# Kernel optimization log

Hardware: AMD Instinct MI355X
Metric: run time of the kernel (lower is better)

The kernel has to match this reference:

```python
import jax, jax.numpy as jnp
import numpy as np

B, L, D = 2, 2048, 2048
HQ, HKV = 32, 8
HD = D // HQ            # 64
G = HQ // HKV           # 4


def setup_inputs() -> dict:
    key = jax.random.key(0)
    ks = jax.random.split(key, 9)
    s = 1.0 / np.sqrt(D)
    return {
        "x": jax.random.normal(ks[0], (B, L, D), jnp.float32),
        "Wq": jax.random.normal(ks[1], (D, HQ * HD), jnp.float32) * s,
        "bq": jnp.zeros((HQ * HD,), jnp.float32),
        "Wk": jax.random.normal(ks[2], (D, HKV * HD), jnp.float32) * s,
        "bk": jnp.zeros((HKV * HD,), jnp.float32),
        "Wv": jax.random.normal(ks[3], (D, HKV * HD), jnp.float32) * s,
        "bv": jnp.zeros((HKV * HD,), jnp.float32),
        "Wo": jax.random.normal(ks[4], (HQ * HD, D), jnp.float32) * s,
        "bo": jnp.zeros((D,), jnp.float32),
    }


def reference(x, Wq, bq, Wk, bk, Wv, bv, Wo, bo):
    # projections
    q = x @ Wq + bq                                   # [B, L, HQ*HD]
    k = x @ Wk + bk                                   # [B, L, HKV*HD]
    v = x @ Wv + bv
    # split heads; group q heads by kv head: [B, HKV, G, L, HD]
    q = q.reshape(B, L, HKV, G, HD).transpose(0, 2, 3, 1, 4)
    k = k.reshape(B, L, HKV, HD).transpose(0, 2, 1, 3)   # [B, HKV, L, HD]
    v = v.reshape(B, L, HKV, HD).transpose(0, 2, 1, 3)
    scale = 1.0 / np.sqrt(HD)
    # scores [B, HKV, G, Lq, Lk] -- same math as repeat_kv + matmul
    scores = jnp.einsum('bhgqd,bhkd->bhgqk', q, k) * scale
    attn = jax.nn.softmax(scores, axis=-1)
    ctx = jnp.einsum('bhgqk,bhkd->bhgqd', attn, v)       # [B, HKV, G, L, HD]
    # merge heads back to [B, L, HQ*HD]
    ctx = ctx.transpose(0, 3, 1, 2, 4).reshape(B, L, HQ * HD)
    return ctx @ Wo + bo
```

## Files before the change

### kernel.cpp

```cpp
#include <hip/hip_runtime.h>
#include <cstdint>
#include <cstring>


#define L_SEQ 2048
#define D_MODEL 2048
#define M_ROWS 4096
#define KV_COLS 512
#define ATTN_SCALE 0.18033688011112042f

typedef __bf16 bf16x8 __attribute__((ext_vector_type(8)));
typedef float f32x4 __attribute__((ext_vector_type(4)));
typedef float f32x16 __attribute__((ext_vector_type(16)));

__device__ __forceinline__ f32x4 zero4() {
    f32x4 v; v[0] = 0.f; v[1] = 0.f; v[2] = 0.f; v[3] = 0.f; return v;
}

__device__ __forceinline__ unsigned short f2bf(float x) {
    unsigned u = __builtin_bit_cast(unsigned, x);
    u = (u + 0x7FFFu + ((u >> 16) & 1u)) >> 16;
    return (unsigned short)u;
}

__device__ __forceinline__ unsigned pk_bf16(float a, float b) {
#if __has_builtin(__builtin_amdgcn_cvt_pk_bf16_f32)
    typedef __bf16 bf16x2 __attribute__((ext_vector_type(2)));
    bf16x2 r = __builtin_amdgcn_cvt_pk_bf16_f32(a, b);
    return __builtin_bit_cast(unsigned, r);
#else
    return (unsigned)f2bf(a) | ((unsigned)f2bf(b) << 16);
#endif
}

__device__ __forceinline__ f32x4 mfma16(uint4 a, uint4 b, f32x4 c) {
    return __builtin_amdgcn_mfma_f32_16x16x32_bf16(
        __builtin_bit_cast(bf16x8, a), __builtin_bit_cast(bf16x8, b), c, 0, 0, 0);
}
__device__ __forceinline__ f32x16 mfma32(uint4 a, uint4 b, f32x16 c) {
    return __builtin_amdgcn_mfma_f32_32x32x16_bf16(
        __builtin_bit_cast(bf16x8, a), __builtin_bit_cast(bf16x8, b), c, 0, 0, 0);
}

__device__ __forceinline__ void gl_lds16(const unsigned short* g, unsigned short* l) {
    __builtin_amdgcn_global_load_lds(
        (const __attribute__((address_space(1))) unsigned int*)g,
        (__attribute__((address_space(3))) unsigned int*)l, 16, 0, 0);
}

#if __has_builtin(__builtin_amdgcn_exp2f)
#define EXP2F(x) __builtin_amdgcn_exp2f(x)
#else
#define EXP2F(x) exp2f(x)
#endif

__device__ __forceinline__ void permswap32(unsigned& a, unsigned& b) {
    asm("v_permlane32_swap_b32 %0, %1" : "+v"(a), "+v"(b));
}


__global__ __launch_bounds__(256) void cast_x_kernel(const float* __restrict__ in,
                                                     unsigned short* __restrict__ out,
                                                     int n4) {
    int i = blockIdx.x * 256 + threadIdx.x;
    if (i >= n4) return;
    float4 v = ((const float4*)in)[i];
    uint2 o;
    o.x = pk_bf16(v.x, v.y);
    o.y = pk_bf16(v.z, v.w);
    ((uint2*)out)[i] = o;
}

__global__ __launch_bounds__(256) void transpose_cast_kernel(const float* __restrict__ in,
                                                             unsigned short* __restrict__ out,
                                                             int N, int row_off) {
    __shared__ float tile[32][33];
    const int n0 = blockIdx.x * 32, k0 = blockIdx.y * 32;
    const int tc = threadIdx.x & 31, tr = threadIdx.x >> 5;
#pragma unroll
    for (int i = 0; i < 4; ++i)
        tile[tr + i * 8][tc] = in[(size_t)(k0 + tr + i * 8) * N + n0 + tc];
    __syncthreads();
#pragma unroll
    for (int i = 0; i < 4; ++i)
        out[(size_t)(row_off + n0 + tr + i * 8) * 2048 + k0 + tc] = f2bf(tile[tc][tr + i * 8]);
}

__global__ __launch_bounds__(256) void transpose_v_kernel(const unsigned short* __restrict__ Vb,
                                                          unsigned short* __restrict__ Vt) {
    __shared__ unsigned short tile[32][33];
    const int c0 = blockIdx.x * 32, l0 = blockIdx.y * 32, b = blockIdx.z;
    const int tc = threadIdx.x & 31, tr = threadIdx.x >> 5;
#pragma unroll
    for (int i = 0; i < 4; ++i)
        tile[tr + i * 8][tc] = Vb[(size_t)(b * 2048 + l0 + tr + i * 8) * KV_COLS + c0 + tc];
    __syncthreads();
#pragma unroll
    for (int i = 0; i < 4; ++i)
        Vt[(size_t)(b * 512 + c0 + tr + i * 8) * 2048 + l0 + tc] = tile[tc][tr + i * 8];
}


__device__ __forceinline__ void gemm_ring_core(const unsigned short* __restrict__ A,
                                               const unsigned short* __restrict__ Bt,
                                               int arow0, int brow0,
                                               char* smem, f32x4 acc[4][2]) {
    const int tid = threadIdx.x;
    const int w = tid >> 6, lane = tid & 63;
    const int wm = w >> 2, wn = w & 3;
    const int lr = lane & 15, lg = lane >> 4;
    const int rr = lane >> 3, cp = lane & 7;

#pragma unroll
    for (int i = 0; i < 4; ++i)
#pragma unroll
        for (int j = 0; j < 2; ++j) acc[i][j] = zero4();

    auto stage = [&](int kt, int slot) {
        char* base = smem + slot * 32768;
        const int k8 = kt * 64 + ((cp ^ rr) * 8);
#pragma unroll
        for (int s = 0; s < 2; ++s) {
            const int c = w * 2 + s;
            gl_lds16(A + (size_t)(arow0 + c * 8 + rr) * 2048 + k8,
                     (unsigned short*)(base + c * 1024));
            gl_lds16(Bt + (size_t)(brow0 + c * 8 + rr) * 2048 + k8,
                     (unsigned short*)(base + 16384 + c * 1024));
        }
    };

    stage(0, 0);
    stage(1, 1);

    for (int t = 0; t < 32; ++t) {
        if (t < 31) asm volatile("s_waitcnt vmcnt(4)" ::: "memory");
        else        asm volatile("s_waitcnt vmcnt(0)" ::: "memory");
        __builtin_amdgcn_s_barrier();
        asm volatile("" ::: "memory");

        if (t <= 29) stage(t + 2, (t + 2) % 3);

        const char* Ab = smem + (t % 3) * 32768;
        const char* Bb = Ab + 16384;

        uint4 fa[4][2], fb[2][2];
#pragma unroll
        for (int mi = 0; mi < 4; ++mi) {
            const int row = wm * 64 + mi * 16 + lr;
#pragma unroll
            for (int ks = 0; ks < 2; ++ks)
                fa[mi][ks] = *(const uint4*)(Ab + row * 128 +
                                             (((ks * 4 + lg) ^ (lr & 7)) * 16));
        }
#pragma unroll
        for (int nj = 0; nj < 2; ++nj) {
            const int row = wn * 32 + nj * 16 + lr;
#pragma unroll
            for (int ks = 0; ks < 2; ++ks)
                fb[nj][ks] = *(const uint4*)(Bb + row * 128 +
                                             (((ks * 4 + lg) ^ (lr & 7)) * 16));
        }
        __builtin_amdgcn_s_setprio(1);
#pragma unroll
        for (int mi = 0; mi < 4; ++mi)
#pragma unroll
            for (int nj = 0; nj < 2; ++nj) {
                acc[mi][nj] = mfma16(fa[mi][0], fb[nj][0], acc[mi][nj]);
                acc[mi][nj] = mfma16(fa[mi][1], fb[nj][1], acc[mi][nj]);
            }
        __builtin_amdgcn_s_setprio(0);
    }
}

__global__ __launch_bounds__(512, 1) void gemm_qkv_kernel(
    const unsigned short* __restrict__ Xb, const unsigned short* __restrict__ Wt,
    const float* __restrict__ bq, const float* __restrict__ bk, const float* __restrict__ bv,
    unsigned short* __restrict__ Qb, unsigned short* __restrict__ Kb,
    unsigned short* __restrict__ Vb) {
    __shared__ __align__(16) char smem[98304];

    const int mb = blockIdx.x, nb = blockIdx.y;
    f32x4 acc[4][2];
    gemm_ring_core(Xb, Wt, mb * 128, nb * 128, smem, acc);

    const int tid = threadIdx.x;
    const int w = tid >> 6, lane = tid & 63;
    const int wm = w >> 2, wn = w & 3;
    const int lr = lane & 15, lg = lane >> 4;

    const int nbase = nb * 128;
    unsigned short* outp; int ldo, noff; const float* bias; float scale;
    if (nbase < 2048)      { outp = Qb; ldo = 2048; noff = 0;    bias = bq; scale = 1.f; }
    else if (nbase < 2560) { outp = Kb; ldo = 512;  noff = 2048; bias = bk; scale = ATTN_SCALE; }
    else                   { outp = Vb; ldo = 512;  noff = 2560; bias = bv; scale = 1.f; }

    __syncthreads();
    float* ep = (float*)(smem + (size_t)w * 8192);
#pragma unroll
    for (int mi = 0; mi < 4; ++mi)
#pragma unroll
        for (int nj = 0; nj < 2; ++nj)
#pragma unroll
            for (int r = 0; r < 4; ++r)
                ep[(mi * 16 + lg * 4 + r) * 32 + nj * 16 + lr] = acc[mi][nj][r];
    __builtin_amdgcn_s_waitcnt(0);
#pragma unroll
    for (int p = 0; p < 4; ++p) {
        const int row = p * 16 + (lane >> 2);
        const int cc = lane & 3;
        const float* v = ep + row * 32 + cc * 8;
        const float4 va = *(const float4*)v;
        const float4 vb2 = *(const float4*)(v + 4);
        const int nloc = nbase + wn * 32 + cc * 8 - noff;
        const float4 b0 = *(const float4*)(bias + nloc);
        const float4 b1 = *(const float4*)(bias + nloc + 4);
        uint4 o;
        o.x = pk_bf16((va.x + b0.x) * scale, (va.y + b0.y) * scale);
        o.y = pk_bf16((va.z + b0.z) * scale, (va.w + b0.w) * scale);
        o.z = pk_bf16((vb2.x + b1.x) * scale, (vb2.y + b1.y) * scale);
        o.w = pk_bf16((vb2.z + b1.z) * scale, (vb2.w + b1.w) * scale);
        *(uint4*)(outp + (size_t)(mb * 128 + wm * 64 + row) * ldo + nloc) = o;
    }
}

__global__ __launch_bounds__(512, 1) void gemm_out_kernel(
    const unsigned short* __restrict__ Cb, const unsigned short* __restrict__ Wot,
    const float* __restrict__ bo, float* __restrict__ out) {
    __shared__ __align__(16) char smem[98304];

    const int mb = blockIdx.x, nb = blockIdx.y;
    f32x4 acc[4][2];
    gemm_ring_core(Cb, Wot, mb * 128, nb * 128, smem, acc);

    const int tid = threadIdx.x;
    const int w = tid >> 6, lane = tid & 63;
    const int wm = w >> 2, wn = w & 3;
    const int lr = lane & 15, lg = lane >> 4;

#pragma unroll
    for (int mi = 0; mi < 4; ++mi) {
        const int mrow = mb * 128 + wm * 64 + mi * 16 + lg * 4;
#pragma unroll
        for (int nj = 0; nj < 2; ++nj) {
            const int ncol = nb * 128 + wn * 32 + nj * 16 + lr;
            const float bb = bo[ncol];
#pragma unroll
            for (int r = 0; r < 4; ++r)
                out[(size_t)(mrow + r) * 2048 + ncol] = acc[mi][nj][r] + bb;
        }
    }
}


__global__ __launch_bounds__(512, 2) void attn_kernel(const unsigned short* __restrict__ Qb,
                                                      const unsigned short* __restrict__ Kb,
                                                      const unsigned short* __restrict__ Vtg,
                                                      unsigned short* __restrict__ ctx) {
    __shared__ __align__(16) unsigned short smem[32768];

    const int qt = blockIdx.x, hq = blockIdx.y, b = blockIdx.z;
    const int kvh = hq >> 2;
    const int tid = threadIdx.x;
    const int w = tid >> 6, lane = tid & 63;
    const int l31 = lane & 31, h = lane >> 5;

    const int qbase = qt * 512 + w * 64;
    uint4 qf[2][4];
#pragma unroll
    for (int u = 0; u < 2; ++u) {
        const unsigned short* qp =
            Qb + (size_t)(b * L_SEQ + qbase + u * 32 + l31) * 2048 + hq * 64;
#pragma unroll
        for (int dh = 0; dh < 4; ++dh)
            qf[u][dh] = *(const uint4*)(qp + dh * 16 + h * 8);
    }

    f32x16 o00, o01, o10, o11;
#pragma unroll
    for (int r = 0; r < 16; ++r) { o00[r] = 0.f; o01[r] = 0.f; o10[r] = 0.f; o11[r] = 0.f; }
    float l_acc0 = 0.f, l_acc1 = 0.f;

    const size_t kbase = (size_t)(b * L_SEQ) * KV_COLS + kvh * 64;
    const size_t vbase = (size_t)((b * 8 + kvh) * 64) * 2048;

    const int rrk = lane >> 3, cpk = lane & 7;
    const int drv = lane >> 4, cpv = lane & 15;

    unsigned short* ksC = smem;
    unsigned short* vtC = smem + 8192;
    unsigned short* ksN = smem + 16384;
    unsigned short* vtN = smem + 24576;

    auto stage = [&](int T, unsigned short* KS, unsigned short* VT) {
        const int k0s = T * 128;
#pragma unroll
        for (int s = 0; s < 2; ++s) {
            const int blk = w * 2 + s;
            gl_lds16(Kb + kbase + (size_t)(k0s + blk * 8 + rrk) * KV_COLS + ((cpk ^ rrk) * 8),
                     KS + blk * 512);
            const int d = blk * 4 + drv;
            gl_lds16(Vtg + vbase + (size_t)d * 2048 + k0s + ((cpv ^ (d & 15)) * 8),
                     VT + blk * 512);
        }
    };

    stage(0, ksC, vtC);
    __syncthreads();

    for (int t = 0; t < 16; ++t) {
        if (t < 15) stage(t + 1, ksN, vtN);

#pragma unroll
        for (int c = 0; c < 4; ++c) {
            uint4 kf[4];
#pragma unroll
            for (int dh = 0; dh < 4; ++dh)
                kf[dh] = *(const uint4*)&ksC[(c * 32 + l31) * 64 +
                                             (((dh * 2 + h) ^ (l31 & 7)) * 8)];
            unsigned E0[4][2], E1[4][2];
#pragma unroll
            for (int u = 0; u < 2; ++u) {
                f32x16 s;
#pragma unroll
                for (int r = 0; r < 16; ++r) s[r] = 0.f;
                __builtin_amdgcn_s_setprio(1);
#pragma unroll
                for (int dh = 0; dh < 4; ++dh) s = mfma32(kf[dh], qf[u][dh], s);
                __builtin_amdgcn_s_setprio(0);
                float lsum = 0.f;
#pragma unroll
                for (int g = 0; g < 4; ++g) {
                    float e0 = EXP2F(s[4 * g + 0]);
                    float e1 = EXP2F(s[4 * g + 1]);
                    float e2 = EXP2F(s[4 * g + 2]);
                    float e3 = EXP2F(s[4 * g + 3]);
                    lsum += (e0 + e1) + (e2 + e3);
                    if (u == 0) { E0[g][0] = pk_bf16(e0, e1); E0[g][1] = pk_bf16(e2, e3); }
                    else        { E1[g][0] = pk_bf16(e0, e1); E1[g][1] = pk_bf16(e2, e3); }
                }
                if (u == 0) l_acc0 += lsum; else l_acc1 += lsum;
            }
#pragma unroll
            for (int tau = 0; tau < 2; ++tau) {
                const int pos = ((c * 4 + tau * 2 + h) ^ (l31 & 15)) * 8;
                uint4 vf0 = *(const uint4*)&vtC[(size_t)l31 * 128 + pos];
                uint4 vf1 = *(const uint4*)&vtC[(size_t)(32 + l31) * 128 + pos];
                {
                    unsigned x0 = E0[2 * tau][0], z0 = E0[2 * tau + 1][0];
                    unsigned x1 = E0[2 * tau][1], z1 = E0[2 * tau + 1][1];
                    permswap32(x0, z0);
                    permswap32(x1, z1);
                    uint4 pf; pf.x = x0; pf.y = x1; pf.z = z0; pf.w = z1;
                    __builtin_amdgcn_s_setprio(1);
                    o00 = mfma32(vf0, pf, o00);
                    o01 = mfma32(vf1, pf, o01);
                    __builtin_amdgcn_s_setprio(0);
                }
                {
                    unsigned x0 = E1[2 * tau][0], z0 = E1[2 * tau + 1][0];
                    unsigned x1 = E1[2 * tau][1], z1 = E1[2 * tau + 1][1];
                    permswap32(x0, z0);
                    permswap32(x1, z1);
                    uint4 pf; pf.x = x0; pf.y = x1; pf.z = z0; pf.w = z1;
                    __builtin_amdgcn_s_setprio(1);
                    o10 = mfma32(vf0, pf, o10);
                    o11 = mfma32(vf1, pf, o11);
                    __builtin_amdgcn_s_setprio(0);
                }
            }
        }

        __syncthreads();
        unsigned short* tk = ksC; ksC = ksN; ksN = tk;
        unsigned short* tv = vtC; vtC = vtN; vtN = tv;
    }

    unsigned* ep = (unsigned*)smem + w * 1088;
#pragma unroll
    for (int u = 0; u < 2; ++u) {
        const float la = u ? l_acc1 : l_acc0;
        const float l_tot = la + __shfl_xor(la, 32, 64);
        const float rl = 1.f / l_tot;
#pragma unroll
        for (int dt = 0; dt < 2; ++dt) {
            const f32x16& o = u ? (dt ? o11 : o10) : (dt ? o01 : o00);
#pragma unroll
            for (int g = 0; g < 4; ++g)
#pragma unroll
                for (int p = 0; p < 2; ++p) {
                    const int dv = dt * 16 + 4 * g + 2 * h + p;
                    ep[l31 * 34 + dv] =
                        pk_bf16(o[4 * g + 2 * p] * rl, o[4 * g + 2 * p + 1] * rl);
                }
        }
        __builtin_amdgcn_s_waitcnt(0);
#pragma unroll
        for (int p = 0; p < 4; ++p) {
            const int qr = (lane >> 3) + p * 8;
            const int cch = lane & 7;
            uint4 vv = *(const uint4*)((const unsigned short*)ep + qr * 68 + cch * 8);
            *(uint4*)(ctx + (size_t)(b * L_SEQ + qbase + u * 32 + qr) * 2048 +
                      hq * 64 + cch * 8) = vv;
        }
        __builtin_amdgcn_s_waitcnt(0);
    }
}


extern "C" void kernel_launch(void* const* d_in, const int* in_sizes, int n_in,
                              void* d_out, int out_size, void* d_ws, size_t ws_size,
                              hipStream_t stream) {
    const float* x  = (const float*)d_in[0];
    const float* Wq = (const float*)d_in[1];
    const float* bq = (const float*)d_in[2];
    const float* Wk = (const float*)d_in[3];
    const float* bk = (const float*)d_in[4];
    const float* Wv = (const float*)d_in[5];
    const float* bv = (const float*)d_in[6];
    const float* Wo = (const float*)d_in[7];
    const float* bo = (const float*)d_in[8];
    float* out = (float*)d_out;

    char* ws = (char*)d_ws;
    size_t off = 0;
    auto alloc = [&](size_t bytes) {
        char* p = ws + off;
        off += (bytes + 255) & ~(size_t)255;
        return p;
    };
    unsigned short* Wqkvt = (unsigned short*)alloc((size_t)3072 * 2048 * 2);
    unsigned short* Wot   = (unsigned short*)alloc((size_t)2048 * 2048 * 2);
    unsigned short* Xb    = (unsigned short*)alloc((size_t)M_ROWS * 2048 * 2);
    unsigned short* Qb    = (unsigned short*)alloc((size_t)M_ROWS * 2048 * 2);
    unsigned short* Kb    = (unsigned short*)alloc((size_t)M_ROWS * KV_COLS * 2);
    unsigned short* Vb    = (unsigned short*)alloc((size_t)M_ROWS * KV_COLS * 2);
    unsigned short* Vt    = (unsigned short*)alloc((size_t)M_ROWS * KV_COLS * 2);
    unsigned short* Cb    = Xb;

    cast_x_kernel<<<(M_ROWS * 2048 / 4 + 255) / 256, 256, 0, stream>>>(x, Xb,
                                                                       M_ROWS * 2048 / 4);
    transpose_cast_kernel<<<dim3(64, 64), 256, 0, stream>>>(Wq, Wqkvt, 2048, 0);
    transpose_cast_kernel<<<dim3(16, 64), 256, 0, stream>>>(Wk, Wqkvt, 512, 2048);
    transpose_cast_kernel<<<dim3(16, 64), 256, 0, stream>>>(Wv, Wqkvt, 512, 2560);
    transpose_cast_kernel<<<dim3(64, 64), 256, 0, stream>>>(Wo, Wot, 2048, 0);
    gemm_qkv_kernel<<<dim3(32, 24), 512, 0, stream>>>(Xb, Wqkvt, bq, bk, bv, Qb, Kb, Vb);
    transpose_v_kernel<<<dim3(16, 64, 2), 256, 0, stream>>>(Vb, Vt);
    attn_kernel<<<dim3(4, 32, 2), 512, 0, stream>>>(Qb, Kb, Vt, Cb);
    gemm_out_kernel<<<dim3(32, 16), 512, 0, stream>>>(Cb, Wot, bo, out);
}
```

Measured before the change: 310.5 us.

## Restructure GEMM core to 4 waves with 64x64 warp tiles and K=32 stages

The shared GEMM core moves from 8 waves, each computing a 64x32 sub-tile over K=64 stages, to 4 waves of 256 threads, each computing a 64x64 sub-tile over K=32 stages. The LDS ring drops from 96KB to 48KB, with a new row-pair swizzled layout, so up to three blocks can be resident per CU. The aim is to raise per-wave register reuse of loaded fragments and improve occupancy and latency hiding. In exchange there are twice as many barriers per K sweep, more accumulator registers per wave, and the QKV epilogue now runs in two passes.

Result: slower. 321.0 us (+3.4%).

```diff
diff --git a/kernel.cpp b/kernel.cpp
--- a/kernel.cpp
+++ b/kernel.cpp
@@ -104,88 +104,86 @@
 __device__ __forceinline__ void gemm_ring_core(const unsigned short* __restrict__ A,
                                                const unsigned short* __restrict__ Bt,
                                                int arow0, int brow0,
-                                               char* smem, f32x4 acc[4][2]) {
+                                               char* smem, f32x4 acc[4][4]) {
     const int tid = threadIdx.x;
     const int w = tid >> 6, lane = tid & 63;
-    const int wm = w >> 2, wn = w & 3;
+    const int wm = w >> 1, wn = w & 1;
     const int lr = lane & 15, lg = lane >> 4;
-    const int rr = lane >> 3, cp = lane & 7;
+    const int srl = lane >> 3, cs = lane & 7;
 
 #pragma unroll
     for (int i = 0; i < 4; ++i)
 #pragma unroll
-        for (int j = 0; j < 2; ++j) acc[i][j] = zero4();
+        for (int j = 0; j < 4; ++j) acc[i][j] = zero4();
 
     auto stage = [&](int kt, int slot) {
-        char* base = smem + slot * 32768;
-        const int k8 = kt * 64 + ((cp ^ rr) * 8);
+        char* base = smem + slot * 16384;
 #pragma unroll
         for (int s = 0; s < 2; ++s) {
-            const int c = w * 2 + s;
-            gl_lds16(A + (size_t)(arow0 + c * 8 + rr) * 2048 + k8,
-                     (unsigned short*)(base + c * 1024));
-            gl_lds16(Bt + (size_t)(brow0 + c * 8 + rr) * 2048 + k8,
-                     (unsigned short*)(base + 16384 + c * 1024));
+            const int srb = w * 16 + s * 8;
+            const int sr = srb + srl;
+            const int gc = cs ^ (sr & 7);
+            const size_t goff = (size_t)(sr * 2 + (gc >> 2)) * 2048 + kt * 32 + (gc & 3) * 8;
+            gl_lds16(A + (size_t)arow0 * 2048 + goff,
+                     (unsigned short*)(base + srb * 128));
+            gl_lds16(Bt + (size_t)brow0 * 2048 + goff,
+                     (unsigned short*)(base + 8192 + srb * 128));
         }
     };
 
     stage(0, 0);
     stage(1, 1);
 
-    for (int t = 0; t < 32; ++t) {
-        if (t < 31) asm volatile("s_waitcnt vmcnt(4)" ::: "memory");
+    for (int t = 0; t < 64; ++t) {
+        if (t < 63) asm volatile("s_waitcnt vmcnt(4)" ::: "memory");
         else        asm volatile("s_waitcnt vmcnt(0)" ::: "memory");
         __builtin_amdgcn_s_barrier();
         asm volatile("" ::: "memory");
 
-        if (t <= 29) stage(t + 2, (t + 2) % 3);
-
-        const char* Ab = smem + (t % 3) * 32768;
-        const char* Bb = Ab + 16384;
-
-        uint4 fa[4][2], fb[2][2];
+        if (t <= 61) stage(t + 2, (t + 2) % 3);
+
+        const char* Ab = smem + (t % 3) * 16384;
+        const char* Bb = Ab + 8192;
+
+        uint4 fa[4], fb[4];
 #pragma unroll
         for (int mi = 0; mi < 4; ++mi) {
-            const int row = wm * 64 + mi * 16 + lr;
-#pragma unroll
-            for (int ks = 0; ks < 2; ++ks)
-                fa[mi][ks] = *(const uint4*)(Ab + row * 128 +
-                                             (((ks * 4 + lg) ^ (lr & 7)) * 16));
-        }
-#pragma unroll
-        for (int nj = 0; nj < 2; ++nj) {
-            const int row = wn * 32 + nj * 16 + lr;
-#pragma unroll
-            for (int ks = 0; ks < 2; ++ks)
-                fb[nj][ks] = *(const uint4*)(Bb + row * 128 +
-                                             (((ks * 4 + lg) ^ (lr & 7)) * 16));
+            const int R = wm * 64 + mi * 16 + lr;
+            const int sr = R >> 1;
+            const int ph = ((R & 1) * 4 + lg) ^ (sr & 7);
+            fa[mi] = *(const uint4*)(Ab + sr * 128 + ph * 16);
+        }
+#pragma unroll
+        for (int nj = 0; nj < 4; ++nj) {
+            const int R = wn * 64 + nj * 16 + lr;
+            const int sr = R >> 1;
+            const int ph = ((R & 1) * 4 + lg) ^ (sr & 7);
+            fb[nj] = *(const uint4*)(Bb + sr * 128 + ph * 16);
         }
         __builtin_amdgcn_s_setprio(1);
 #pragma unroll
         for (int mi = 0; mi < 4; ++mi)
 #pragma unroll
-            for (int nj = 0; nj < 2; ++nj) {
-                acc[mi][nj] = mfma16(fa[mi][0], fb[nj][0], acc[mi][nj]);
-                acc[mi][nj] = mfma16(fa[mi][1], fb[nj][1], acc[mi][nj]);
-            }
+            for (int nj = 0; nj < 4; ++nj)
+                acc[mi][nj] = mfma16(fa[mi], fb[nj], acc[mi][nj]);
         __builtin_amdgcn_s_setprio(0);
     }
 }
 
-__global__ __launch_bounds__(512, 1) void gemm_qkv_kernel(
+__global__ __launch_bounds__(256, 3) void gemm_qkv_kernel(
     const unsigned short* __restrict__ Xb, const unsigned short* __restrict__ Wt,
     const float* __restrict__ bq, const float* __restrict__ bk, const float* __restrict__ bv,
     unsigned short* __restrict__ Qb, unsigned short* __restrict__ Kb,
     unsigned short* __restrict__ Vb) {
-    __shared__ __align__(16) char smem[98304];
+    __shared__ __align__(16) char smem[49152];
 
     const int mb = blockIdx.x, nb = blockIdx.y;
-    f32x4 acc[4][2];
+    f32x4 acc[4][4];
     gemm_ring_core(Xb, Wt, mb * 128, nb * 128, smem, acc);
 
     const int tid = threadIdx.x;
     const int w = tid >> 6, lane = tid & 63;
-    const int wm = w >> 2, wn = w & 3;
+    const int wm = w >> 1, wn = w & 1;
     const int lr = lane & 15, lg = lane >> 4;
 
     const int nbase = nb * 128;
@@ -195,54 +193,59 @@
     else                   { outp = Vb; ldo = 512;  noff = 2560; bias = bv; scale = 1.f; }
 
     __syncthreads();
-    float* ep = (float*)(smem + (size_t)w * 8192);
-#pragma unroll
-    for (int mi = 0; mi < 4; ++mi)
-#pragma unroll
-        for (int nj = 0; nj < 2; ++nj)
-#pragma unroll
-            for (int r = 0; r < 4; ++r)
-                ep[(mi * 16 + lg * 4 + r) * 32 + nj * 16 + lr] = acc[mi][nj][r];
-    __builtin_amdgcn_s_waitcnt(0);
-#pragma unroll
-    for (int p = 0; p < 4; ++p) {
-        const int row = p * 16 + (lane >> 2);
-        const int cc = lane & 3;
-        const float* v = ep + row * 32 + cc * 8;
-        const float4 va = *(const float4*)v;
-        const float4 vb2 = *(const float4*)(v + 4);
-        const int nloc = nbase + wn * 32 + cc * 8 - noff;
-        const float4 b0 = *(const float4*)(bias + nloc);
-        const float4 b1 = *(const float4*)(bias + nloc + 4);
-        uint4 o;
-        o.x = pk_bf16((va.x + b0.x) * scale, (va.y + b0.y) * scale);
-        o.y = pk_bf16((va.z + b0.z) * scale, (va.w + b0.w) * scale);
-        o.z = pk_bf16((vb2.x + b1.x) * scale, (vb2.y + b1.y) * scale);
-        o.w = pk_bf16((vb2.z + b1.z) * scale, (vb2.w + b1.w) * scale);
-        *(uint4*)(outp + (size_t)(mb * 128 + wm * 64 + row) * ldo + nloc) = o;
-    }
-}
-
-__global__ __launch_bounds__(512, 1) void gemm_out_kernel(
+    float* ep = (float*)(smem + (size_t)w * 12288);
+#pragma unroll
+    for (int pass = 0; pass < 2; ++pass) {
+#pragma unroll
+        for (int mi = 0; mi < 4; ++mi)
+#pragma unroll
+            for (int njl = 0; njl < 2; ++njl)
+#pragma unroll
+                for (int r = 0; r < 4; ++r)
+                    ep[(mi * 16 + lg * 4 + r) * 32 + njl * 16 + lr] =
+                        acc[mi][pass * 2 + njl][r];
+        __builtin_amdgcn_s_waitcnt(0);
+#pragma unroll
+        for (int p2 = 0; p2 < 4; ++p2) {
+            const int row = p2 * 16 + (lane >> 2);
+            const int cc = lane & 3;
+            const float* v = ep + row * 32 + cc * 8;
+            const float4 va = *(const float4*)v;
+            const float4 vb2 = *(const float4*)(v + 4);
+            const int nloc = nbase + wn * 64 + pass * 32 + cc * 8 - noff;
+            const float4 b0 = *(const float4*)(bias + nloc);
+            const float4 b1 = *(const float4*)(bias + nloc + 4);
+            uint4 o;
+            o.x = pk_bf16((va.x + b0.x) * scale, (va.y + b0.y) * scale);
+            o.y = pk_bf16((va.z + b0.z) * scale, (va.w + b0.w) * scale);
+            o.z = pk_bf16((vb2.x + b1.x) * scale, (vb2.y + b1.y) * scale);
+            o.w = pk_bf16((vb2.z + b1.z) * scale, (vb2.w + b1.w) * scale);
+            *(uint4*)(outp + (size_t)(mb * 128 + wm * 64 + row) * ldo + nloc) = o;
+        }
+        __builtin_amdgcn_s_waitcnt(0);
+    }
+}
+
+__global__ __launch_bounds__(256, 3) void gemm_out_kernel(
     const unsigned short* __restrict__ Cb, const unsigned short* __restrict__ Wot,
     const float* __restrict__ bo, float* __restrict__ out) {
-    __shared__ __align__(16) char smem[98304];
+    __shared__ __align__(16) char smem[49152];
 
     const int mb = blockIdx.x, nb = blockIdx.y;
-    f32x4 acc[4][2];
+    f32x4 acc[4][4];
     gemm_ring_core(Cb, Wot, mb * 128, nb * 128, smem, acc);
 
     const int tid = threadIdx.x;
     const int w = tid >> 6, lane = tid & 63;
-    const int wm = w >> 2, wn = w & 3;
+    const int wm = w >> 1, wn = w & 1;
     const int lr = lane & 15, lg = lane >> 4;
 
 #pragma unroll
     for (int mi = 0; mi < 4; ++mi) {
         const int mrow = mb * 128 + wm * 64 + mi * 16 + lg * 4;
 #pragma unroll
-        for (int nj = 0; nj < 2; ++nj) {
-            const int ncol = nb * 128 + wn * 32 + nj * 16 + lr;
+        for (int nj = 0; nj < 4; ++nj) {
+            const int ncol = nb * 128 + wn * 64 + nj * 16 + lr;
             const float bb = bo[ncol];
 #pragma unroll
             for (int r = 0; r < 4; ++r)
@@ -443,8 +446,8 @@
     transpose_cast_kernel<<<dim3(16, 64), 256, 0, stream>>>(Wk, Wqkvt, 512, 2048);
     transpose_cast_kernel<<<dim3(16, 64), 256, 0, stream>>>(Wv, Wqkvt, 512, 2560);
     transpose_cast_kernel<<<dim3(64, 64), 256, 0, stream>>>(Wo, Wot, 2048, 0);
-    gemm_qkv_kernel<<<dim3(32, 24), 512, 0, stream>>>(Xb, Wqkvt, bq, bk, bv, Qb, Kb, Vb);
+    gemm_qkv_kernel<<<dim3(32, 24), 256, 0, stream>>>(Xb, Wqkvt, bq, bk, bv, Qb, Kb, Vb);
     transpose_v_kernel<<<dim3(16, 64, 2), 256, 0, stream>>>(Vb, Vt);
     attn_kernel<<<dim3(4, 32, 2), 512, 0, stream>>>(Qb, Kb, Vt, Cb);
-    gemm_out_kernel<<<dim3(32, 16), 512, 0, stream>>>(Cb, Wot, bo, out);
-}
+    gemm_out_kernel<<<dim3(32, 16), 256, 0, stream>>>(Cb, Wot, bo, out);
+}
```
